# Optimization experiments

Measured on AMD Instinct MI355X. Metric: run time of the kernel, lower is better.

## Reference

```python
import jax, jax.numpy as jnp
import numpy as np
from jax import lax

BN_EPS = 1e-5

def _conv(x, w, groups=1, pad=0):
    return lax.conv_general_dilated(
        x, w, window_strides=(1, 1), padding=[(pad, pad), (pad, pad)],
        dimension_numbers=('NCHW', 'OIHW', 'NCHW'), feature_group_count=groups)

def _gather2d(imgf, yi, xi, H, W):
    # imgf: [B,C,H*W] flattened image; yi, xi: [B,C,H,W] int32 corner indices
    valid = (yi >= 0) & (yi < H) & (xi >= 0) & (xi < W)
    yc = jnp.clip(yi, 0, H - 1)
    xc = jnp.clip(xi, 0, W - 1)
    idx = (yc * W + xc).reshape(imgf.shape[0], imgf.shape[1], -1)
    v = jnp.take_along_axis(imgf, idx, axis=2).reshape(yi.shape)
    return jnp.where(valid, v, 0.0)

def _bilinear_sample(img, y, x):
    # img: [B,C,H,W]; y, x: [B,C,H,W] float sample coords (zero outside)
    B, C, H, W = img.shape
    imgf = img.reshape(B, C, H * W)
    y0 = jnp.floor(y)
    x0 = jnp.floor(x)
    wy = y - y0  # weight for y1 corner
    wx = x - x0
    y0i = y0.astype(jnp.int32); y1i = y0i + 1
    x0i = x0.astype(jnp.int32); x1i = x0i + 1
    v00 = _gather2d(imgf, y0i, x0i, H, W)
    v01 = _gather2d(imgf, y0i, x1i, H, W)
    v10 = _gather2d(imgf, y1i, x0i, H, W)
    v11 = _gather2d(imgf, y1i, x1i, H, W)
    return ((1 - wy) * (1 - wx) * v00 + (1 - wy) * wx * v01
            + wy * (1 - wx) * v10 + wy * wx * v11)

def setup_inputs() -> dict:
    key = jax.random.key(0)
    ks = jax.random.split(key, 6)
    B, C, OC, H, W = 4, 64, 64, 256, 256
    return {
        'x': jax.random.normal(ks[0], (B, C, H, W), jnp.float32),
        'dw_weight': jax.random.normal(ks[1], (C, 1, 3, 3), jnp.float32) * 0.2,
        'pw_weight': jax.random.normal(ks[2], (3 * C, C, 1, 1), jnp.float32) * 0.1,
        'weight': jax.random.normal(ks[3], (OC, C, 1, 1), jnp.float32) * 0.1,
        'bias': jax.random.normal(ks[4], (OC,), jnp.float32) * 0.1,
        'gamma': jnp.ones((OC,), jnp.float32),
        'beta': jnp.zeros((OC,), jnp.float32),
    }

def reference(x, dw_weight, pw_weight, weight, bias, gamma, beta):
    B, C, H, W = x.shape
    # DWConv2d: depthwise 3x3 (pad 1) then pointwise 1x1 -> 3C channels
    om = _conv(_conv(x, dw_weight, groups=C, pad=1), pw_weight)
    offset_y = om[:, :C]
    offset_x = om[:, C:2 * C]
    modulator = 2.0 * jax.nn.sigmoid(om[:, 2 * C:])
    max_off = max(H, W) // 4
    offset = jnp.clip(jnp.concatenate([offset_y, offset_x], axis=1), -max_off, max_off)
    # torchvision deform_conv2d layout: [B, og*2, H, W] interleaved (y, x) per offset group
    off = offset.reshape(B, C, 2, H, W)
    hh = jnp.arange(H, dtype=x.dtype)[:, None]
    ww = jnp.arange(W, dtype=x.dtype)[None, :]
    sy = hh + off[:, :, 0]  # [B,C,H,W]
    sx = ww + off[:, :, 1]
    sampled = _bilinear_sample(x, sy, sx) * modulator
    w2 = weight.reshape(weight.shape[0], C)  # 1x1 kernel -> [OC, C]
    out = jnp.einsum('oc,bchw->bohw', w2, sampled) + bias[None, :, None, None]
    # BatchNorm2d (training-mode batch stats) + exact GELU
    mean = out.mean(axis=(0, 2, 3), keepdims=True)
    var = out.var(axis=(0, 2, 3), keepdims=True)
    out = (out - mean) * lax.rsqrt(var + BN_EPS)
    out = out * gamma[None, :, None, None] + beta[None, :, None, None]
    return jax.nn.gelu(out, approximate=False)
```

## Files before the change

kernel.cpp:

```cpp
#include <hip/hip_runtime.h>

#define B_  4
#define C_  64
#define H_  256
#define W_  256
#define HW_ 65536
#define NPIX_ (B_*HW_)
#define NELEM_ (B_*C_*HW_)

#define OMS 200
#define TS  72

typedef __attribute__((ext_vector_type(8))) short short8;
typedef __attribute__((ext_vector_type(4))) float floatx4;
typedef __attribute__((ext_vector_type(2))) __fp16 h2f;

static __device__ __forceinline__ unsigned short f2bf(float f){
  unsigned u = __float_as_uint(f);
  u += 0x7fff + ((u >> 16) & 1);
  return (unsigned short)(u >> 16);
}
static __device__ __forceinline__ float bf2f(unsigned short s){
  return __uint_as_float(((unsigned)s) << 16);
}
static __device__ __forceinline__ unsigned pack2(float a, float b){
  return (unsigned)f2bf(a) | ((unsigned)f2bf(b) << 16);
}

__global__ __launch_bounds__(256) void k_setup(
    const float* __restrict__ pw, const float* __restrict__ w2,
    unsigned short* __restrict__ wB, float* __restrict__ stats0)
{
  int tid = threadIdx.x;
  if (blockIdx.x < 64){
    int i = blockIdx.x*256 + tid;
    wB[i] = f2bf(i < 12288 ? pw[i] : w2[i - 12288]);
  } else {
#pragma unroll
    for (int k = 0; k < 16; ++k) stats0[k*256 + tid] = 0.f;
  }
}

__global__ __launch_bounds__(256, 4) void k_fuse(
    const float* __restrict__ x,
    const float* __restrict__ dwW,
    const unsigned short* __restrict__ pwB,
    const unsigned short* __restrict__ w2B,
    unsigned short* __restrict__ outB,
    float* __restrict__ gsumS,
    float* __restrict__ gsqS)
{
  __shared__ __align__(16) char lds[34816];
  unsigned short* T  = (unsigned short*)lds;
  unsigned short* OM = (unsigned short*)(lds + 9216);
  float* red1 = (float*)(lds + 9216);
  float* red2 = (float*)(lds + 10240);

  int tid = threadIdx.x;
  int bid = ((blockIdx.x & 7) << 9) + (blockIdx.x >> 3);
  int b    = bid >> 10;
  int tile = bid & 1023;
  int h    = tile >> 2;
  int w0   = (tile & 3) << 6;
  int p  = tid & 63;
  int cg = tid >> 6;
  int wg = w0 + p;

  {
    int rm = (h > 0   ? h-1 : 0) << 8;
    int r0 = h << 8;
    int rp = (h < 255 ? h+1 : 255) << 8;
    float vm = (h > 0)   ? 1.f : 0.f;
    float vp = (h < 255) ? 1.f : 0.f;
    int st = min(max(wg - 1, 0), 253);
    int d  = wg - st;
    bool d0 = (d == 0), d2 = (d == 2);
    int om = (rm + st) << 2;
    int oc = (r0 + st) << 2;
    int op = (rp + st) << 2;

    const char* plane0 = (const char*)(x + ((size_t)(b*C_ + cg*16) << 16));

    unsigned pk[8];
#pragma unroll
    for (int ib = 0; ib < 4; ++ib){
      float3 v[4][3];
#pragma unroll
      for (int j = 0; j < 4; ++j){
        const char* pl = plane0 + (((size_t)(ib*4 + j)) << 18);
        __builtin_memcpy(&v[j][0], pl + om, 12);
        __builtin_memcpy(&v[j][1], pl + oc, 12);
        __builtin_memcpy(&v[j][2], pl + op, 12);
      }
      __builtin_amdgcn_sched_barrier(0);
#pragma unroll
      for (int j = 0; j < 4; ++j){
        int i = ib*4 + j;
        int c = cg*16 + i;
        const float* wp = dwW + c*9;
        float acc = 0.f;
#pragma unroll
        for (int r = 0; r < 3; ++r){
          float3 f = v[j][r];
          float xl = d0 ? 0.f : (d2 ? f.y : f.x);
          float xc = d0 ? f.x : (d2 ? f.z : f.y);
          float xr = d2 ? 0.f : (d0 ? f.y : f.z);
          float rowscale = (r == 0) ? vm : (r == 2 ? vp : 1.f);
          acc += rowscale * (wp[r*3+0]*xl + wp[r*3+1]*xc + wp[r*3+2]*xr);
        }
        unsigned short bv = f2bf(acc);
        if (i & 1) pk[i>>1] |= ((unsigned)bv << 16);
        else       pk[i>>1]  = (unsigned)bv;
      }
    }
    uint4 u0; u0.x = pk[0]; u0.y = pk[1]; u0.z = pk[2]; u0.w = pk[3];
    uint4 u1; u1.x = pk[4]; u1.y = pk[5]; u1.z = pk[6]; u1.w = pk[7];
    *(uint4*)(T + p*TS + cg*16)     = u0;
    *(uint4*)(T + p*TS + cg*16 + 8) = u1;
  }
  __syncthreads();

  int wv = tid >> 6, lane = tid & 63;
  int mrow = lane & 15, q = lane >> 4;
  int pxw = bid*64 + wv*16;

  short8 bfrag[2];
#pragma unroll
  for (int kb = 0; kb < 2; ++kb)
    bfrag[kb] = *(const short8*)(T + (wv*16 + mrow)*TS + kb*32 + q*8);

  floatx4 acc[12];
#pragma unroll
  for (int mt = 0; mt < 12; ++mt) acc[mt] = (floatx4){0.f,0.f,0.f,0.f};
#pragma unroll
  for (int kb = 0; kb < 2; ++kb)
#pragma unroll
    for (int mt = 0; mt < 12; ++mt){
      short8 af = *(const short8*)(pwB + (mt*16 + mrow)*64 + kb*32 + q*8);
      acc[mt] = __builtin_amdgcn_mfma_f32_16x16x32_bf16(af, bfrag[kb], acc[mt], 0, 0, 0);
    }

  {
    int omrow = (wv*16 + mrow)*OMS;
#pragma unroll
    for (int mt = 0; mt < 12; ++mt){
      uint2 u; u.x = pack2(acc[mt][0], acc[mt][1]); u.y = pack2(acc[mt][2], acc[mt][3]);
      *(uint2*)(OM + omrow + mt*16 + q*4) = u;
    }
  }
  __syncthreads();

  unsigned pk[8];
  {
    float hf = (float)h, wf = (float)(w0 + p);
    const char* xbyte = (const char*)(x + ((size_t)(b*C_ + cg*16) << 16));

#pragma unroll
    for (int half = 0; half < 2; ++half){
      const uint4* ob = (const uint4*)(OM + p*OMS + cg*32 + half*16);
      uint4 oA = ob[0], oB = ob[1];
      uint4 mv = *(const uint4*)(OM + p*OMS + 128 + cg*16 + half*8);
      unsigned pr[8] = {oA.x,oA.y,oA.z,oA.w, oB.x,oB.y,oB.z,oB.w};
      unsigned md4[4] = {mv.x,mv.y,mv.z,mv.w};

      h2f wrv[8], wcv[8];
      unsigned ad0[8], ad1[8];

#pragma unroll
      for (int i = 0; i < 8; ++i){
        unsigned pair = pr[i];
        float oy = __uint_as_float(pair << 16);
        float ox = __uint_as_float(pair & 0xffff0000u);
        float mm = __uint_as_float((i & 1) ? (md4[i>>1] & 0xffff0000u)
                                           : (md4[i>>1] << 16));
        float mod = 2.f * __builtin_amdgcn_rcpf(1.f + __expf(-mm));
        oy = fminf(fmaxf(oy, -64.f), 64.f);
        ox = fminf(fmaxf(ox, -64.f), 64.f);
        float sy = hf + oy, sx = wf + ox;
        float y0f = floorf(sy), x0f = floorf(sx);
        float wy = sy - y0f, wxr = sx - x0f;
        int y0 = (int)y0f, x0 = (int)x0f;
        int yc0 = min(max(y0,     0), 255);
        int yc1 = min(max(y0 + 1, 0), 255);
        int xc  = min(max(x0, 0), 254);
        bool y0v = ((unsigned)y0       < 256u);
        bool y1v = ((unsigned)(y0 + 1) < 256u);
        bool x0v = ((unsigned)x0       < 256u);
        bool x1v = ((unsigned)(x0 + 1) < 256u);
        bool x0lo = (x0 == xc);
        float r0 = y0v ? (1.f - wy) * mod : 0.f;
        float r1 = y1v ? wy * mod : 0.f;
        float c0w = x0v ? (1.f - wxr) : 0.f;
        float c1w = x1v ? wxr : 0.f;
        float cA = x0lo ? c0w : c1w;
        float cB = x0lo ? c1w : c0w;
        wrv[i] = __builtin_amdgcn_cvt_pkrtz(r0, r1);
        wcv[i] = __builtin_amdgcn_cvt_pkrtz(cA, cB);
        unsigned cb = ((unsigned)(half*8 + i)) << 18;
        ad0[i] = cb + ((unsigned)yc0 << 10) + ((unsigned)xc << 2);
        ad1[i] = cb + ((unsigned)yc1 << 10) + ((unsigned)xc << 2);
      }

      float2 pu0[8], pu1[8];
#pragma unroll
      for (int i = 0; i < 8; ++i){
        __builtin_memcpy(&pu0[i], xbyte + ad0[i], 8);
        __builtin_memcpy(&pu1[i], xbyte + ad1[i], 8);
      }
      __builtin_amdgcn_sched_barrier(0);

#pragma unroll
      for (int i = 0; i < 8; ++i){
        int ci = half*8 + i;
        float cA = (float)wcv[i].x, cB = (float)wcv[i].y;
        float r0 = (float)wrv[i].x, r1 = (float)wrv[i].y;
        float sres = r0*(cA*pu0[i].x + cB*pu0[i].y)
                   + r1*(cA*pu1[i].x + cB*pu1[i].y);
        unsigned short bv = f2bf(sres);
        if (ci & 1) pk[ci>>1] |= ((unsigned)bv << 16);
        else        pk[ci>>1]  = (unsigned)bv;
      }
    }
  }
  __syncthreads();

  {
    uint4 u0; u0.x = pk[0]; u0.y = pk[1]; u0.z = pk[2]; u0.w = pk[3];
    uint4 u1; u1.x = pk[4]; u1.y = pk[5]; u1.z = pk[6]; u1.w = pk[7];
    *(uint4*)(T + p*TS + cg*16)     = u0;
    *(uint4*)(T + p*TS + cg*16 + 8) = u1;
  }
  __syncthreads();

  short8 a2[2];
#pragma unroll
  for (int kb = 0; kb < 2; ++kb)
    a2[kb] = *(const short8*)(T + (wv*16 + mrow)*TS + kb*32 + q*8);

  floatx4 acc2[4];
#pragma unroll
  for (int nt = 0; nt < 4; ++nt) acc2[nt] = (floatx4){0.f,0.f,0.f,0.f};
#pragma unroll
  for (int kb = 0; kb < 2; ++kb)
#pragma unroll
    for (int nt = 0; nt < 4; ++nt){
      short8 bf = *(const short8*)(w2B + (nt*16 + mrow)*64 + kb*32 + q*8);
      acc2[nt] = __builtin_amdgcn_mfma_f32_16x16x32_bf16(a2[kb], bf, acc2[nt], 0, 0, 0);
    }

  int bb  = pxw >> 16;
  int hw0 = pxw & (HW_-1);
#pragma unroll
  for (int nt = 0; nt < 4; ++nt){
    int och = nt*16 + mrow;
    float a0 = acc2[nt][0], a1 = acc2[nt][1], a2v = acc2[nt][2], a3 = acc2[nt][3];
    uint2 u; u.x = pack2(a0, a1); u.y = pack2(a2v, a3);
    *(uint2*)(outB + ((size_t)(bb*C_ + och) << 16) + hw0 + q*4) = u;
    float s1 = a0 + a1 + a2v + a3;
    float s2 = a0*a0 + a1*a1 + a2v*a2v + a3*a3;
    s1 += __shfl_xor(s1, 16, 64);  s2 += __shfl_xor(s2, 16, 64);
    s1 += __shfl_xor(s1, 32, 64);  s2 += __shfl_xor(s2, 32, 64);
    if (q == 0){ red1[wv*64 + och] = s1; red2[wv*64 + och] = s2; }
  }
  __syncthreads();
  if (tid < 64){
    float t1 = red1[tid] + red1[64+tid] + red1[128+tid] + red1[192+tid];
    float t2 = red2[tid] + red2[64+tid] + red2[128+tid] + red2[192+tid];
    int slot = blockIdx.x & 31;
    atomicAdd(&gsumS[slot*64 + tid], t1);
    atomicAdd(&gsqS[slot*64 + tid], t2);
  }
}

static __device__ __forceinline__ float gelu1(float a){
  float u = a*a;
  float wv = fmaf(u*a, -0.0713548162726f, a * -1.5957691216f);
  return a * __builtin_amdgcn_rcpf(1.f + __expf(wv));
}

__global__ __launch_bounds__(256) void k_bn_gelu(
    const uint4* __restrict__ outB4,
    const float* __restrict__ gsumS,
    const float* __restrict__ gsqS,
    const float* __restrict__ gamma,
    const float* __restrict__ beta,
    float4* __restrict__ y4)
{
  int i = blockIdx.x*256 + threadIdx.x;
  int och = (i >> 13) & 63;
  float s1 = 0.f, s2 = 0.f;
#pragma unroll
  for (int s = 0; s < 32; ++s){ s1 += gsumS[s*64 + och]; s2 += gsqS[s*64 + och]; }
  float mean = s1 * (1.f/(float)NPIX_);
  float var  = s2 * (1.f/(float)NPIX_) - mean*mean;
  float sc = gamma[och] * rsqrtf(var + 1e-5f);
  float sh = beta[och] - mean*sc;

  uint4 u = outB4[i];
  float e[8];
  e[0] = bf2f((unsigned short)(u.x & 0xffffu)); e[1] = bf2f((unsigned short)(u.x >> 16));
  e[2] = bf2f((unsigned short)(u.y & 0xffffu)); e[3] = bf2f((unsigned short)(u.y >> 16));
  e[4] = bf2f((unsigned short)(u.z & 0xffffu)); e[5] = bf2f((unsigned short)(u.z >> 16));
  e[6] = bf2f((unsigned short)(u.w & 0xffffu)); e[7] = bf2f((unsigned short)(u.w >> 16));
  float4 o0, o1;
  o0.x = gelu1(fmaf(e[0], sc, sh));
  o0.y = gelu1(fmaf(e[1], sc, sh));
  o0.z = gelu1(fmaf(e[2], sc, sh));
  o0.w = gelu1(fmaf(e[3], sc, sh));
  o1.x = gelu1(fmaf(e[4], sc, sh));
  o1.y = gelu1(fmaf(e[5], sc, sh));
  o1.z = gelu1(fmaf(e[6], sc, sh));
  o1.w = gelu1(fmaf(e[7], sc, sh));
  y4[2*i]   = o0;
  y4[2*i+1] = o1;
}

extern "C" void kernel_launch(void* const* d_in, const int* in_sizes, int n_in,
                              void* d_out, int out_size, void* d_ws, size_t ws_size,
                              hipStream_t stream)
{
  (void)in_sizes; (void)n_in; (void)out_size; (void)ws_size;
  const float* x     = (const float*)d_in[0];
  const float* dw    = (const float*)d_in[1];
  const float* pw    = (const float*)d_in[2];
  const float* w2    = (const float*)d_in[3];
  const float* gamma = (const float*)d_in[5];
  const float* beta  = (const float*)d_in[6];

  char* ws = (char*)d_ws;
  unsigned short* outB  = (unsigned short*)ws;
  float*          stats = (float*)(ws + 33554432);
  float* gsumS = stats;
  float* gsqS  = stats + 2048;
  unsigned short* wB  = (unsigned short*)(ws + 33570816);
  unsigned short* pwB = wB;
  unsigned short* w2B = wB + 12288;

  k_setup   <<<65, 256, 0, stream>>>(pw, w2, wB, stats);
  k_fuse    <<<NPIX_/64, 256, 0, stream>>>(x, dw, pwB, w2B, outB, gsumS, gsqS);
  k_bn_gelu <<<NELEM_/8/256, 256, 0, stream>>>((const uint4*)outB, gsumS, gsqS,
                                               gamma, beta, (float4*)d_out);
}
```

Baseline: 258.6 us.

## Compute depthwise conv directly into MFMA fragments and batch BN-GELU per block

The depthwise 3x3 stage now has each lane compute exactly the channels and pixel its MFMA B-fragment needs. This removes the LDS staging buffer T and the __syncthreads between depthwise and pointwise, which shrinks LDS and raises the occupancy hint from 4 to 5 blocks. The BN-GELU kernel now handles 1024 vec8 elements per block, with a per-channel stat reduction done once by wave shuffles instead of 64 scalar loads per thread. The cost is a less coalesced x access pattern in the depthwise load and more per-lane weight loads.

```diff
diff --git a/kernel.cpp b/kernel.cpp
--- a/kernel.cpp
+++ b/kernel.cpp
@@ -41,7 +41,7 @@
   }
 }
 
-__global__ __launch_bounds__(256, 4) void k_fuse(
+__global__ __launch_bounds__(256, 5) void k_fuse(
     const float* __restrict__ x,
     const float* __restrict__ dwW,
     const unsigned short* __restrict__ pwB,
@@ -50,9 +50,9 @@
     float* __restrict__ gsumS,
     float* __restrict__ gsqS)
 {
-  __shared__ __align__(16) char lds[34816];
+  __shared__ __align__(16) char lds[25600];
+  unsigned short* OM = (unsigned short*)lds;
   unsigned short* T  = (unsigned short*)lds;
-  unsigned short* OM = (unsigned short*)(lds + 9216);
   float* red1 = (float*)(lds + 9216);
   float* red2 = (float*)(lds + 10240);
 
@@ -64,70 +64,72 @@
   int w0   = (tile & 3) << 6;
   int p  = tid & 63;
   int cg = tid >> 6;
-  int wg = w0 + p;
-
+
+  int wv = tid >> 6, lane = tid & 63;
+  int mrow = lane & 15, q = lane >> 4;
+  int pxw = bid*64 + wv*16;
+
+  short8 bfrag[2];
   {
+    int col = w0 + wv*16 + mrow;
     int rm = (h > 0   ? h-1 : 0) << 8;
     int r0 = h << 8;
     int rp = (h < 255 ? h+1 : 255) << 8;
     float vm = (h > 0)   ? 1.f : 0.f;
     float vp = (h < 255) ? 1.f : 0.f;
-    int st = min(max(wg - 1, 0), 253);
-    int d  = wg - st;
+    int st = min(max(col - 1, 0), 253);
+    int d  = col - st;
     bool d0 = (d == 0), d2 = (d == 2);
     int om = (rm + st) << 2;
     int oc = (r0 + st) << 2;
     int op = (rp + st) << 2;
 
-    const char* plane0 = (const char*)(x + ((size_t)(b*C_ + cg*16) << 16));
-
-    unsigned pk[8];
-#pragma unroll
-    for (int ib = 0; ib < 4; ++ib){
-      float3 v[4][3];
-#pragma unroll
-      for (int j = 0; j < 4; ++j){
-        const char* pl = plane0 + (((size_t)(ib*4 + j)) << 18);
-        __builtin_memcpy(&v[j][0], pl + om, 12);
-        __builtin_memcpy(&v[j][1], pl + oc, 12);
-        __builtin_memcpy(&v[j][2], pl + op, 12);
+    const char* xbase = (const char*)(x + ((size_t)(b*C_) << 16));
+
+#pragma unroll
+    for (int kb = 0; kb < 2; ++kb){
+      union { unsigned u[4]; short8 s8; } cv;
+#pragma unroll
+      for (int sb = 0; sb < 2; ++sb){
+        float3 v[4][3];
+        float3 wr[4][3];
+#pragma unroll
+        for (int j = 0; j < 4; ++j){
+          int c = kb*32 + q*8 + sb*4 + j;
+          const char* pl = xbase + (((size_t)c) << 18);
+          __builtin_memcpy(&v[j][0], pl + om, 12);
+          __builtin_memcpy(&v[j][1], pl + oc, 12);
+          __builtin_memcpy(&v[j][2], pl + op, 12);
+          const float* wp = dwW + c*9;
+          __builtin_memcpy(&wr[j][0], wp,     12);
+          __builtin_memcpy(&wr[j][1], wp + 3, 12);
+          __builtin_memcpy(&wr[j][2], wp + 6, 12);
+        }
+        __builtin_amdgcn_sched_barrier(0);
+        unsigned pkv[2];
+#pragma unroll
+        for (int j = 0; j < 4; ++j){
+          float acc = 0.f;
+#pragma unroll
+          for (int r = 0; r < 3; ++r){
+            float3 f = v[j][r];
+            float3 wf = wr[j][r];
+            float xl = d0 ? 0.f : (d2 ? f.y : f.x);
+            float xc = d0 ? f.x : (d2 ? f.z : f.y);
+            float xr = d2 ? 0.f : (d0 ? f.y : f.z);
+            float rowscale = (r == 0) ? vm : (r == 2 ? vp : 1.f);
+            acc += rowscale * (wf.x*xl + wf.y*xc + wf.z*xr);
+          }
+          unsigned short bv = f2bf(acc);
+          if (j & 1) pkv[j>>1] |= ((unsigned)bv << 16);
+          else       pkv[j>>1]  = (unsigned)bv;
+        }
+        cv.u[sb*2]     = pkv[0];
+        cv.u[sb*2 + 1] = pkv[1];
       }
-      __builtin_amdgcn_sched_barrier(0);
-#pragma unroll
-      for (int j = 0; j < 4; ++j){
-        int i = ib*4 + j;
-        int c = cg*16 + i;
-        const float* wp = dwW + c*9;
-        float acc = 0.f;
-#pragma unroll
-        for (int r = 0; r < 3; ++r){
-          float3 f = v[j][r];
-          float xl = d0 ? 0.f : (d2 ? f.y : f.x);
-          float xc = d0 ? f.x : (d2 ? f.z : f.y);
-          float xr = d2 ? 0.f : (d0 ? f.y : f.z);
-          float rowscale = (r == 0) ? vm : (r == 2 ? vp : 1.f);
-          acc += rowscale * (wp[r*3+0]*xl + wp[r*3+1]*xc + wp[r*3+2]*xr);
-        }
-        unsigned short bv = f2bf(acc);
-        if (i & 1) pk[i>>1] |= ((unsigned)bv << 16);
-        else       pk[i>>1]  = (unsigned)bv;
-      }
-    }
-    uint4 u0; u0.x = pk[0]; u0.y = pk[1]; u0.z = pk[2]; u0.w = pk[3];
-    uint4 u1; u1.x = pk[4]; u1.y = pk[5]; u1.z = pk[6]; u1.w = pk[7];
-    *(uint4*)(T + p*TS + cg*16)     = u0;
-    *(uint4*)(T + p*TS + cg*16 + 8) = u1;
-  }
-  __syncthreads();
-
-  int wv = tid >> 6, lane = tid & 63;
-  int mrow = lane & 15, q = lane >> 4;
-  int pxw = bid*64 + wv*16;
-
-  short8 bfrag[2];
-#pragma unroll
-  for (int kb = 0; kb < 2; ++kb)
-    bfrag[kb] = *(const short8*)(T + (wv*16 + mrow)*TS + kb*32 + q*8);
+      bfrag[kb] = cv.s8;
+    }
+  }
 
   floatx4 acc[12];
 #pragma unroll
@@ -286,33 +288,43 @@
     const float* __restrict__ beta,
     float4* __restrict__ y4)
 {
-  int i = blockIdx.x*256 + threadIdx.x;
-  int och = (i >> 13) & 63;
-  float s1 = 0.f, s2 = 0.f;
-#pragma unroll
-  for (int s = 0; s < 32; ++s){ s1 += gsumS[s*64 + och]; s2 += gsqS[s*64 + och]; }
+  int tid = threadIdx.x;
+  int och = (blockIdx.x >> 3) & 63;
+  int l = tid & 63;
+  float part = (l < 32) ? gsumS[l*64 + och] : gsqS[(l-32)*64 + och];
+  part += __shfl_xor(part, 1, 64);
+  part += __shfl_xor(part, 2, 64);
+  part += __shfl_xor(part, 4, 64);
+  part += __shfl_xor(part, 8, 64);
+  part += __shfl_xor(part, 16, 64);
+  float s1 = __shfl(part, 0, 64);
+  float s2 = __shfl(part, 32, 64);
   float mean = s1 * (1.f/(float)NPIX_);
   float var  = s2 * (1.f/(float)NPIX_) - mean*mean;
   float sc = gamma[och] * rsqrtf(var + 1e-5f);
   float sh = beta[och] - mean*sc;
 
-  uint4 u = outB4[i];
-  float e[8];
-  e[0] = bf2f((unsigned short)(u.x & 0xffffu)); e[1] = bf2f((unsigned short)(u.x >> 16));
-  e[2] = bf2f((unsigned short)(u.y & 0xffffu)); e[3] = bf2f((unsigned short)(u.y >> 16));
-  e[4] = bf2f((unsigned short)(u.z & 0xffffu)); e[5] = bf2f((unsigned short)(u.z >> 16));
-  e[6] = bf2f((unsigned short)(u.w & 0xffffu)); e[7] = bf2f((unsigned short)(u.w >> 16));
-  float4 o0, o1;
-  o0.x = gelu1(fmaf(e[0], sc, sh));
-  o0.y = gelu1(fmaf(e[1], sc, sh));
-  o0.z = gelu1(fmaf(e[2], sc, sh));
-  o0.w = gelu1(fmaf(e[3], sc, sh));
-  o1.x = gelu1(fmaf(e[4], sc, sh));
-  o1.y = gelu1(fmaf(e[5], sc, sh));
-  o1.z = gelu1(fmaf(e[6], sc, sh));
-  o1.w = gelu1(fmaf(e[7], sc, sh));
-  y4[2*i]   = o0;
-  y4[2*i+1] = o1;
+#pragma unroll
+  for (int it = 0; it < 4; ++it){
+    int i = blockIdx.x*1024 + it*256 + tid;
+    uint4 u = outB4[i];
+    float e[8];
+    e[0] = bf2f((unsigned short)(u.x & 0xffffu)); e[1] = bf2f((unsigned short)(u.x >> 16));
+    e[2] = bf2f((unsigned short)(u.y & 0xffffu)); e[3] = bf2f((unsigned short)(u.y >> 16));
+    e[4] = bf2f((unsigned short)(u.z & 0xffffu)); e[5] = bf2f((unsigned short)(u.z >> 16));
+    e[6] = bf2f((unsigned short)(u.w & 0xffffu)); e[7] = bf2f((unsigned short)(u.w >> 16));
+    float4 o0, o1;
+    o0.x = gelu1(fmaf(e[0], sc, sh));
+    o0.y = gelu1(fmaf(e[1], sc, sh));
+    o0.z = gelu1(fmaf(e[2], sc, sh));
+    o0.w = gelu1(fmaf(e[3], sc, sh));
+    o1.x = gelu1(fmaf(e[4], sc, sh));
+    o1.y = gelu1(fmaf(e[5], sc, sh));
+    o1.z = gelu1(fmaf(e[6], sc, sh));
+    o1.w = gelu1(fmaf(e[7], sc, sh));
+    y4[2*i]   = o0;
+    y4[2*i+1] = o1;
+  }
 }
 
 extern "C" void kernel_launch(void* const* d_in, const int* in_sizes, int n_in,
@@ -338,6 +350,6 @@
 
   k_setup   <<<65, 256, 0, stream>>>(pw, w2, wB, stats);
   k_fuse    <<<NPIX_/64, 256, 0, stream>>>(x, dw, pwB, w2B, outB, gsumS, gsqS);
-  k_bn_gelu <<<NELEM_/8/256, 256, 0, stream>>>((const uint4*)outB, gsumS, gsqS,
-                                               gamma, beta, (float4*)d_out);
-}
+  k_bn_gelu <<<2048, 256, 0, stream>>>((const uint4*)outB, gsumS, gsqS,
+                                       gamma, beta, (float4*)d_out);
+}
```

Result: slower. 285.3 us (+10.3%).
